# Performance work log

Hardware: AMD Instinct MI355X
Metric: run time of the kernel (lower is better)

## Reference

```python
import jax, jax.numpy as jnp
import numpy as np

B, M, K, P = 64, 8, 4, 16  # batch, rx antennas, streams, constellation size
NBPS = 4  # 16-QAM


def _qam_points(nbps):
    # square QAM, unit average energy
    n = 2 ** (nbps // 2)
    pam = 2.0 * np.arange(n) - n + 1.0  # e.g. {-3,-1,1,3}
    re, im = np.meshgrid(pam, pam, indexing='ij')
    pts = (re + 1j * im).reshape(-1)
    pts = pts / np.sqrt(np.mean(np.abs(pts) ** 2))
    return pts.astype(np.complex64)


def _build_vecs(points, k):
    # replicate MaximumLikelihoodDetector._build_vecs: stream 0 varies slowest
    p = points.shape[0]
    grids = np.meshgrid(*([np.arange(p)] * k), indexing='ij')
    idx = np.stack(grids, axis=-1).reshape(-1, k)        # [P^K, K]
    vecs = points[idx]                                   # [P^K, K] complex
    c = np.stack([
        np.stack([np.where(idx[:, j] == pi)[0] for j in range(k)], axis=-1)
        for pi in range(p)
    ], axis=-1)                                          # [P^(K-1), K, P]
    return vecs, c.astype(np.int32)


def setup_inputs() -> dict:
    key = jax.random.key(0)
    ks = jax.random.split(key, 6)
    points = _qam_points(NBPS)
    vecs, c = _build_vecs(points, K)
    yr = jax.random.normal(ks[0], (B, M), jnp.float32)
    yi = jax.random.normal(ks[1], (B, M), jnp.float32)
    hr = jax.random.normal(ks[2], (B, M, K), jnp.float32)
    hi = jax.random.normal(ks[3], (B, M, K), jnp.float32)
    # Hermitian positive-definite noise covariance s = A A^H / M + I
    ar = jax.random.normal(ks[4], (B, M, M), jnp.float32)
    ai = jax.random.normal(ks[5], (B, M, M), jnp.float32)
    a = (ar + 1j * ai).astype(jnp.complex64)
    s = a @ jnp.conj(jnp.swapaxes(a, -1, -2)) / M + jnp.eye(M, dtype=jnp.complex64)
    return {
        'yr': yr, 'yi': yi, 'hr': hr, 'hi': hi,
        'sr': jnp.real(s).astype(jnp.float32), 'si': jnp.imag(s).astype(jnp.float32),
        'vr': jnp.asarray(vecs.real), 'vi': jnp.asarray(vecs.imag),
        'c': jnp.asarray(c),
    }


def reference(yr, yi, hr, hi, sr, si, vr, vi, c):
    y = (yr + 1j * yi).astype(jnp.complex64)          # [B, M]
    h = (hr + 1j * hi).astype(jnp.complex64)          # [B, M, K]
    s = (sr + 1j * si).astype(jnp.complex64)          # [B, M, M]
    vecs = (vr + 1j * vi).astype(jnp.complex64)       # [V, K]
    # whitening: s_inv = inv(cholesky(s))
    L = jnp.linalg.cholesky(s)
    s_inv = jnp.linalg.inv(L)                         # [B, M, M]
    yw = jnp.einsum('bmn,bn->bm', s_inv, y)           # [B, M]
    hw = jnp.einsum('bmn,bnk->bmk', s_inv, h)         # [B, M, K]
    # distances for every candidate symbol vector
    hv = jnp.einsum('bmk,vk->bvm', hw, vecs)          # [B, V, M]
    diff = yw[:, None, :] - hv                        # [B, V, M]
    exponents = -jnp.sum(diff.real ** 2 + diff.imag ** 2, axis=-1)  # [B, V]
    # regroup exponents by (stream, symbol) and reduce (app -> logsumexp)
    exp_g = exponents[:, c]                           # [B, P^(K-1), K, P]
    logits = jax.nn.logsumexp(exp_g, axis=-3)         # [B, K, P]
    return logits
```

## Files before the change

### kernel.cpp

```cpp
#include <hip/hip_runtime.h>
#include <math.h>


__global__ __launch_bounds__(256) void k_main(
    const float* __restrict__ yr, const float* __restrict__ yi,
    const float* __restrict__ hr, const float* __restrict__ hi,
    const float* __restrict__ sr, const float* __restrict__ si,
    const float* __restrict__ vr, const float* __restrict__ vi,
    float* __restrict__ ws, float* __restrict__ out)
{
    __shared__ float sL[8][8][2];
    __shared__ float sDinv[8];
    __shared__ float lyw[8][2];
    __shared__ float lhw[8][4][2];
    __shared__ float tab[4][16][8][2];
    __shared__ float xbuf[16][256];
    __shared__ float pA[256], pB[256], pC[256];
    __shared__ float lmax[48];
    __shared__ float gsum[48];

    const int t = threadIdx.x;
    const int bid = blockIdx.x;
    const int b = bid >> 4, chunk = bid & 15;

    float Lr_[8], Li_[8], a_r[8], a_i[8];
    if (t < 8) {
#pragma unroll
        for (int k = 0; k < 8; ++k) {
            a_r[k] = sr[b * 64 + t * 8 + k];
            a_i[k] = si[b * 64 + t * 8 + k];
        }
    }
#pragma unroll
    for (int j = 0; j < 8; ++j) {
        if (t == j) {
            float d = a_r[j];
#pragma unroll
            for (int k = 0; k < 8; ++k) if (k < j) d -= Lr_[k]*Lr_[k] + Li_[k]*Li_[k];
            float ld = sqrtf(d);
            Lr_[j] = ld; Li_[j] = 0.f;
            sDinv[j] = 1.f / ld;
#pragma unroll
            for (int k = 0; k < 8; ++k) if (k <= j) { sL[j][k][0] = Lr_[k]; sL[j][k][1] = Li_[k]; }
        }
        __syncthreads();
        if (t < 8 && t > j) {
            float cr = a_r[j], ci = a_i[j];
#pragma unroll
            for (int k = 0; k < 8; ++k) if (k < j) {
                cr -= Lr_[k]*sL[j][k][0] + Li_[k]*sL[j][k][1];
                ci -= Li_[k]*sL[j][k][0] - Lr_[k]*sL[j][k][1];
            }
            float inv = sDinv[j];
            Lr_[j] = cr * inv; Li_[j] = ci * inv;
        }
    }
    if (t < 5) {
        float rr[8], ri[8], zr[8], zi[8];
        if (t == 0) {
#pragma unroll
            for (int i = 0; i < 8; ++i) { rr[i] = yr[b*8+i]; ri[i] = yi[b*8+i]; }
        } else {
#pragma unroll
            for (int i = 0; i < 8; ++i) { rr[i] = hr[(b*8+i)*4 + (t-1)]; ri[i] = hi[(b*8+i)*4 + (t-1)]; }
        }
#pragma unroll
        for (int i = 0; i < 8; ++i) {
            float cr = rr[i], ci = ri[i];
#pragma unroll
            for (int k = 0; k < 8; ++k) if (k < i) {
                cr -= sL[i][k][0]*zr[k] - sL[i][k][1]*zi[k];
                ci -= sL[i][k][0]*zi[k] + sL[i][k][1]*zr[k];
            }
            float inv = sDinv[i];
            zr[i] = cr * inv; zi[i] = ci * inv;
            if (t == 0) { lyw[i][0] = zr[i]; lyw[i][1] = zi[i]; }
            else        { lhw[i][t-1][0] = zr[i]; lhw[i][t-1][1] = zi[i]; }
        }
    }
    __syncthreads();

    for (int e = t; e < 512; e += 256) {
        int k = e >> 7, p = (e >> 3) & 15, m = e & 7;
        float hre = lhw[m][k][0], him = lhw[m][k][1];
        float pr = vr[(p << 12) * 4], pim = vi[(p << 12) * 4];
        tab[k][p][m][0] = hre*pr - him*pim;
        tab[k][p][m][1] = hre*pim + him*pr;
    }
    __syncthreads();

    const int i3 = t & 15, i2 = t >> 4;
    float br[8], bi[8];
#pragma unroll
    for (int m = 0; m < 8; ++m) {
        br[m] = tab[0][chunk][m][0] + tab[2][i2][m][0] + tab[3][i3][m][0] - lyw[m][0];
        bi[m] = tab[0][chunk][m][1] + tab[2][i2][m][1] + tab[3][i3][m][1] - lyw[m][1];
    }
#pragma unroll
    for (int s = 0; s < 16; ++s) {
        float acc = 0.f;
#pragma unroll
        for (int m = 0; m < 8; ++m) {
            float dr = br[m] + tab[1][s][m][0];
            float di = bi[m] + tab[1][s][m][1];
            acc += dr*dr + di*di;
        }
        xbuf[s][t] = -acc;
    }
    __syncthreads();

    float vmA = xbuf[0][t];
#pragma unroll
    for (int s = 1; s < 16; ++s) vmA = fmaxf(vmA, xbuf[s][t]);
    pA[t] = vmA;
    float vmB = xbuf[i2][i3];
#pragma unroll
    for (int d2 = 1; d2 < 16; ++d2) vmB = fmaxf(vmB, xbuf[i2][d2*16 + i3]);
    pB[t] = vmB;
    __syncthreads();
    if (t < 16) {
        float v1 = pB[t*16], v2 = pA[t*16], v3 = pA[t];
#pragma unroll
        for (int i = 1; i < 16; ++i) {
            v1 = fmaxf(v1, pB[t*16 + i]);
            v2 = fmaxf(v2, pA[t*16 + i]);
            v3 = fmaxf(v3, pA[t + 16*i]);
        }
        lmax[t] = v1; lmax[16+t] = v2; lmax[32+t] = v3;
    }
    __syncthreads();

    const float M1 = lmax[i2];
    const float M2 = lmax[16 + i2];
    const float M3 = lmax[32 + i3];
    float acc1 = 0.f, acc2 = 0.f, acc3 = 0.f;
#pragma unroll
    for (int s = 0; s < 16; ++s) {
        float v = xbuf[s][t];
        acc2 += __expf(v - M2);
        acc3 += __expf(v - M3);
    }
#pragma unroll
    for (int d2 = 0; d2 < 16; ++d2) {
        float w = xbuf[i2][d2*16 + i3];
        acc1 += __expf(w - M1);
    }
    pA[t] = acc2; pB[t] = acc3; pC[t] = acc1;
    __syncthreads();
    if (t < 16) {
        float s1 = 0.f, s2 = 0.f, s3 = 0.f;
#pragma unroll
        for (int i = 0; i < 16; ++i) {
            s1 += pC[t*16 + i];
            s2 += pA[t*16 + i];
            s3 += pB[t + 16*i];
        }
        gsum[t] = s1; gsum[16+t] = s2; gsum[32+t] = s3;
    }
    __syncthreads();

    if (t < 48) {
        float* w = ws + ((b*48 + t)*16 + chunk)*2;
        w[0] = lmax[t];
        w[1] = gsum[t];
    }
    if (t == 0) {
        float M = lmax[16];
#pragma unroll
        for (int i = 1; i < 16; ++i) M = fmaxf(M, lmax[16+i]);
        float S = 0.f;
#pragma unroll
        for (int i = 0; i < 16; ++i) S += gsum[16+i] * __expf(lmax[16+i] - M);
        out[b*64 + chunk] = logf(S) + M;
    }
}

__global__ __launch_bounds__(256) void k_comb(const float* __restrict__ ws, float* __restrict__ out)
{
    int idx = blockIdx.x * 256 + threadIdx.x;
    if (idx >= 64 * 48) return;
    int b = idx / 48, gi = idx % 48;
    const float* p = ws + (b*48 + gi)*32;
    float M = p[0];
#pragma unroll
    for (int i = 1; i < 16; ++i) M = fmaxf(M, p[2*i]);
    float S = 0.f;
#pragma unroll
    for (int i = 0; i < 16; ++i) S += p[2*i+1] * __expf(p[2*i] - M);
    out[b*64 + 16 + gi] = logf(S) + M;
}

extern "C" void kernel_launch(void* const* d_in, const int* in_sizes, int n_in,
                              void* d_out, int out_size, void* d_ws, size_t ws_size,
                              hipStream_t stream) {
    const float* yr = (const float*)d_in[0];
    const float* yi = (const float*)d_in[1];
    const float* hr = (const float*)d_in[2];
    const float* hi = (const float*)d_in[3];
    const float* sr = (const float*)d_in[4];
    const float* si = (const float*)d_in[5];
    const float* vr = (const float*)d_in[6];
    const float* vi = (const float*)d_in[7];
    float* ws = (float*)d_ws;
    float* out = (float*)d_out;
    hipLaunchKernelGGL(k_main, dim3(1024), dim3(256), 0, stream,
                       yr, yi, hr, hi, sr, si, vr, vi, ws, out);
    hipLaunchKernelGGL(k_comb, dim3(12), dim3(256), 0, stream, ws, out);
}
```

Baseline: 20.36 us.

## Restructure ML detector kernel with wave shuffles, expanded distance, and single-exp logsumexp

Cholesky factorization now runs inside one wavefront and uses lane shuffles instead of block-wide barriers. Distances are computed in expanded form (|b|^2 + |p|^2|h1|^2 + 2Re(b·t1)), so each candidate needs a dot product rather than a full squared difference. All 16 values stay in registers and the max/sum reductions use wave shuffles, so the shared xbuf and most __syncthreads calls are gone. One exp pass against min(M2,M3), rescaled afterwards, replaces the two separate exp loops. The expanded-distance form and the rescaling trick can lose floating-point accuracy or underflow when M2 and M3 are far apart.

```diff
diff --git a/kernel.cpp b/kernel.cpp
--- a/kernel.cpp
+++ b/kernel.cpp
@@ -13,165 +13,211 @@
     __shared__ float sDinv[8];
     __shared__ float lyw[8][2];
     __shared__ float lhw[8][4][2];
-    __shared__ float tab[4][16][8][2];
-    __shared__ float xbuf[16][256];
-    __shared__ float pA[256], pB[256], pC[256];
-    __shared__ float lmax[48];
-    __shared__ float gsum[48];
+    __shared__ float tab[4][8][16][2];
+    __shared__ float pn2b[16];
+    __shared__ float Hn1b;
+    __shared__ float m3w[4][16], s3w[4][16];
+    __shared__ float p1buf[16][16];
+    __shared__ float m1cbuf[16][16];
+    __shared__ float m2buf[16], s2buf[16];
 
     const int t = threadIdx.x;
-    const int bid = blockIdx.x;
-    const int b = bid >> 4, chunk = bid & 15;
-
-    float Lr_[8], Li_[8], a_r[8], a_i[8];
-    if (t < 8) {
-#pragma unroll
-        for (int k = 0; k < 8; ++k) {
-            a_r[k] = sr[b * 64 + t * 8 + k];
-            a_i[k] = si[b * 64 + t * 8 + k];
-        }
-    }
-#pragma unroll
-    for (int j = 0; j < 8; ++j) {
-        if (t == j) {
-            float d = a_r[j];
-#pragma unroll
-            for (int k = 0; k < 8; ++k) if (k < j) d -= Lr_[k]*Lr_[k] + Li_[k]*Li_[k];
-            float ld = sqrtf(d);
-            Lr_[j] = ld; Li_[j] = 0.f;
-            sDinv[j] = 1.f / ld;
-#pragma unroll
-            for (int k = 0; k < 8; ++k) if (k <= j) { sL[j][k][0] = Lr_[k]; sL[j][k][1] = Li_[k]; }
-        }
-        __syncthreads();
-        if (t < 8 && t > j) {
-            float cr = a_r[j], ci = a_i[j];
+    const int b = blockIdx.x >> 4, chunk = blockIdx.x & 15;
+    const int lane = t & 63, wv = t >> 6;
+    const int i3 = t & 15, i2 = t >> 4;
+
+    if (wv == 0) {
+        float ar_[8] = {}, ai_[8] = {}, Lr_[8] = {}, Li_[8] = {};
+        if (lane < 8) {
+#pragma unroll
+            for (int k = 0; k < 8; ++k) {
+                ar_[k] = sr[b * 64 + lane * 8 + k];
+                ai_[k] = si[b * 64 + lane * 8 + k];
+            }
+        }
+        float inv = 0.f;
+#pragma unroll
+        for (int j = 0; j < 8; ++j) {
+            if (lane == j) {
+                float d = ar_[j];
+#pragma unroll
+                for (int k = 0; k < 8; ++k) if (k < j) d -= Lr_[k]*Lr_[k] + Li_[k]*Li_[k];
+                float ld = sqrtf(d);
+                Lr_[j] = ld; Li_[j] = 0.f;
+                inv = 1.f / ld;
+                sDinv[j] = inv;
+            }
+            float invj = __shfl(inv, j);
+            float cr = ar_[j], ci = ai_[j];
 #pragma unroll
             for (int k = 0; k < 8; ++k) if (k < j) {
-                cr -= Lr_[k]*sL[j][k][0] + Li_[k]*sL[j][k][1];
-                ci -= Li_[k]*sL[j][k][0] - Lr_[k]*sL[j][k][1];
-            }
-            float inv = sDinv[j];
-            Lr_[j] = cr * inv; Li_[j] = ci * inv;
-        }
-    }
-    if (t < 5) {
-        float rr[8], ri[8], zr[8], zi[8];
-        if (t == 0) {
-#pragma unroll
-            for (int i = 0; i < 8; ++i) { rr[i] = yr[b*8+i]; ri[i] = yi[b*8+i]; }
-        } else {
-#pragma unroll
-            for (int i = 0; i < 8; ++i) { rr[i] = hr[(b*8+i)*4 + (t-1)]; ri[i] = hi[(b*8+i)*4 + (t-1)]; }
-        }
-#pragma unroll
-        for (int i = 0; i < 8; ++i) {
-            float cr = rr[i], ci = ri[i];
-#pragma unroll
-            for (int k = 0; k < 8; ++k) if (k < i) {
-                cr -= sL[i][k][0]*zr[k] - sL[i][k][1]*zi[k];
-                ci -= sL[i][k][0]*zi[k] + sL[i][k][1]*zr[k];
-            }
-            float inv = sDinv[i];
-            zr[i] = cr * inv; zi[i] = ci * inv;
-            if (t == 0) { lyw[i][0] = zr[i]; lyw[i][1] = zi[i]; }
-            else        { lhw[i][t-1][0] = zr[i]; lhw[i][t-1][1] = zi[i]; }
+                float Ljrk = __shfl(Lr_[k], j);
+                float Ljik = __shfl(Li_[k], j);
+                cr -= Lr_[k]*Ljrk + Li_[k]*Ljik;
+                ci -= Li_[k]*Ljrk - Lr_[k]*Ljik;
+            }
+            if (lane < 8 && lane > j) { Lr_[j] = cr * invj; Li_[j] = ci * invj; }
+        }
+        if (lane < 8) {
+#pragma unroll
+            for (int k = 0; k < 8; ++k) if (k <= lane) { sL[lane][k][0] = Lr_[k]; sL[lane][k][1] = Li_[k]; }
+        }
+        if (lane < 5) {
+            float rr[8], ri[8], zr[8], zi[8];
+            if (lane == 0) {
+#pragma unroll
+                for (int i = 0; i < 8; ++i) { rr[i] = yr[b*8+i]; ri[i] = yi[b*8+i]; }
+            } else {
+#pragma unroll
+                for (int i = 0; i < 8; ++i) { rr[i] = hr[(b*8+i)*4 + (lane-1)]; ri[i] = hi[(b*8+i)*4 + (lane-1)]; }
+            }
+#pragma unroll
+            for (int i = 0; i < 8; ++i) {
+                float cr = rr[i], ci = ri[i];
+#pragma unroll
+                for (int k = 0; k < 8; ++k) if (k < i) {
+                    cr -= sL[i][k][0]*zr[k] - sL[i][k][1]*zi[k];
+                    ci -= sL[i][k][0]*zi[k] + sL[i][k][1]*zr[k];
+                }
+                float dv = sDinv[i];
+                zr[i] = cr * dv; zi[i] = ci * dv;
+                if (lane == 0) { lyw[i][0] = zr[i]; lyw[i][1] = zi[i]; }
+                else           { lhw[i][lane-1][0] = zr[i]; lhw[i][lane-1][1] = zi[i]; }
+            }
+        }
+        {
+            int p = lane & 15;
+            float pr  = vr[(p << 12) * 4];
+            float pim = vi[(p << 12) * 4];
+            if (lane < 16) pn2b[lane] = pr*pr + pim*pim;
+            if (lane == 0) {
+                float hn = 0.f;
+#pragma unroll
+                for (int m = 0; m < 8; ++m) hn += lhw[m][1][0]*lhw[m][1][0] + lhw[m][1][1]*lhw[m][1][1];
+                Hn1b = hn;
+            }
+#pragma unroll
+            for (int it = 0; it < 8; ++it) {
+                int e = lane + it * 64;
+                int k = e >> 7, m = (e >> 4) & 7;
+                float hre = lhw[m][k][0], him = lhw[m][k][1];
+                tab[k][m][p][0] = hre*pr  - him*pim;
+                tab[k][m][p][1] = hre*pim + him*pr;
+            }
         }
     }
     __syncthreads();
 
-    for (int e = t; e < 512; e += 256) {
-        int k = e >> 7, p = (e >> 3) & 15, m = e & 7;
-        float hre = lhw[m][k][0], him = lhw[m][k][1];
-        float pr = vr[(p << 12) * 4], pim = vi[(p << 12) * 4];
-        tab[k][p][m][0] = hre*pr - him*pim;
-        tab[k][p][m][1] = hre*pim + him*pr;
+    float br_[8], bi_[8];
+    float B2 = 0.f;
+#pragma unroll
+    for (int m = 0; m < 8; ++m) {
+        const float2 t0 = *(const float2*)&tab[0][m][chunk][0];
+        const float2 t2 = *(const float2*)&tab[2][m][i2][0];
+        const float2 t3 = *(const float2*)&tab[3][m][i3][0];
+        const float2 yw = *(const float2*)&lyw[m][0];
+        br_[m] = t0.x + t2.x + t3.x - yw.x;
+        bi_[m] = t0.y + t2.y + t3.y - yw.y;
+        B2 = fmaf(br_[m], br_[m], fmaf(bi_[m], bi_[m], B2));
+    }
+    const float Hn1 = Hn1b;
+
+    float x_[16];
+    float vmA = -3.4e38f;
+#pragma unroll
+    for (int s = 0; s < 16; ++s) {
+        float D = 0.f;
+#pragma unroll
+        for (int m = 0; m < 8; ++m) {
+            const float2 t1 = *(const float2*)&tab[1][m][s][0];
+            D = fmaf(br_[m], t1.x, D);
+            D = fmaf(bi_[m], t1.y, D);
+        }
+        float x = fmaf(-2.f, D, -fmaf(pn2b[s], Hn1, B2));
+        x_[s] = x;
+        vmA = fmaxf(vmA, x);
+    }
+
+    float M2 = vmA;
+    M2 = fmaxf(M2, __shfl_xor(M2, 1));
+    M2 = fmaxf(M2, __shfl_xor(M2, 2));
+    M2 = fmaxf(M2, __shfl_xor(M2, 4));
+    M2 = fmaxf(M2, __shfl_xor(M2, 8));
+    float m3p = vmA;
+    m3p = fmaxf(m3p, __shfl_xor(m3p, 16));
+    m3p = fmaxf(m3p, __shfl_xor(m3p, 32));
+    if (lane < 16) m3w[wv][lane] = m3p;
+
+#pragma unroll
+    for (int s = 0; s < 16; ++s) {
+        float rcm = x_[s];
+        rcm = fmaxf(rcm, __shfl_xor(rcm, 1));
+        rcm = fmaxf(rcm, __shfl_xor(rcm, 2));
+        rcm = fmaxf(rcm, __shfl_xor(rcm, 4));
+        rcm = fmaxf(rcm, __shfl_xor(rcm, 8));
+        float e1 = __expf(x_[s] - rcm);
+        e1 += __shfl_xor(e1, 1);
+        e1 += __shfl_xor(e1, 2);
+        e1 += __shfl_xor(e1, 4);
+        e1 += __shfl_xor(e1, 8);
+        if (i3 == 0) { p1buf[s][i2] = e1; m1cbuf[s][i2] = rcm; }
     }
     __syncthreads();
 
-    const int i3 = t & 15, i2 = t >> 4;
-    float br[8], bi[8];
-#pragma unroll
-    for (int m = 0; m < 8; ++m) {
-        br[m] = tab[0][chunk][m][0] + tab[2][i2][m][0] + tab[3][i3][m][0] - lyw[m][0];
-        bi[m] = tab[0][chunk][m][1] + tab[2][i2][m][1] + tab[3][i3][m][1] - lyw[m][1];
-    }
-#pragma unroll
-    for (int s = 0; s < 16; ++s) {
-        float acc = 0.f;
-#pragma unroll
-        for (int m = 0; m < 8; ++m) {
-            float dr = br[m] + tab[1][s][m][0];
-            float di = bi[m] + tab[1][s][m][1];
-            acc += dr*dr + di*di;
-        }
-        xbuf[s][t] = -acc;
+    const float M3 = fmaxf(fmaxf(m3w[0][i3], m3w[1][i3]), fmaxf(m3w[2][i3], m3w[3][i3]));
+    const float Mlo = fminf(M2, M3);
+    float acc = 0.f;
+#pragma unroll
+    for (int s = 0; s < 16; ++s) acc += __expf(x_[s] - Mlo);
+    float acc2 = acc * __expf(Mlo - M2);
+    float acc3 = acc * __expf(Mlo - M3);
+    float S2 = acc2;
+    S2 += __shfl_xor(S2, 1);
+    S2 += __shfl_xor(S2, 2);
+    S2 += __shfl_xor(S2, 4);
+    S2 += __shfl_xor(S2, 8);
+    float s3p = acc3;
+    s3p += __shfl_xor(s3p, 16);
+    s3p += __shfl_xor(s3p, 32);
+    if (lane < 16) s3w[wv][lane] = s3p;
+    if (i3 == 0) {
+        m2buf[i2] = M2; s2buf[i2] = S2;
+        float* w = ws + ((b*48 + 16 + i2)*16 + chunk)*2;
+        w[0] = M2; w[1] = S2;
     }
     __syncthreads();
 
-    float vmA = xbuf[0][t];
-#pragma unroll
-    for (int s = 1; s < 16; ++s) vmA = fmaxf(vmA, xbuf[s][t]);
-    pA[t] = vmA;
-    float vmB = xbuf[i2][i3];
-#pragma unroll
-    for (int d2 = 1; d2 < 16; ++d2) vmB = fmaxf(vmB, xbuf[i2][d2*16 + i3]);
-    pB[t] = vmB;
-    __syncthreads();
+    {
+        float p1v = p1buf[i2][i3];
+        float m1c = m1cbuf[i2][i3];
+        float M1 = m1c;
+        M1 = fmaxf(M1, __shfl_xor(M1, 1));
+        M1 = fmaxf(M1, __shfl_xor(M1, 2));
+        M1 = fmaxf(M1, __shfl_xor(M1, 4));
+        M1 = fmaxf(M1, __shfl_xor(M1, 8));
+        float q = p1v * __expf(m1c - M1);
+        q += __shfl_xor(q, 1);
+        q += __shfl_xor(q, 2);
+        q += __shfl_xor(q, 4);
+        q += __shfl_xor(q, 8);
+        if (i3 == 0) {
+            float* w = ws + ((b*48 + i2)*16 + chunk)*2;
+            w[0] = M1; w[1] = q;
+        }
+    }
     if (t < 16) {
-        float v1 = pB[t*16], v2 = pA[t*16], v3 = pA[t];
-#pragma unroll
-        for (int i = 1; i < 16; ++i) {
-            v1 = fmaxf(v1, pB[t*16 + i]);
-            v2 = fmaxf(v2, pA[t*16 + i]);
-            v3 = fmaxf(v3, pA[t + 16*i]);
-        }
-        lmax[t] = v1; lmax[16+t] = v2; lmax[32+t] = v3;
-    }
-    __syncthreads();
-
-    const float M1 = lmax[i2];
-    const float M2 = lmax[16 + i2];
-    const float M3 = lmax[32 + i3];
-    float acc1 = 0.f, acc2 = 0.f, acc3 = 0.f;
-#pragma unroll
-    for (int s = 0; s < 16; ++s) {
-        float v = xbuf[s][t];
-        acc2 += __expf(v - M2);
-        acc3 += __expf(v - M3);
-    }
-#pragma unroll
-    for (int d2 = 0; d2 < 16; ++d2) {
-        float w = xbuf[i2][d2*16 + i3];
-        acc1 += __expf(w - M1);
-    }
-    pA[t] = acc2; pB[t] = acc3; pC[t] = acc1;
-    __syncthreads();
-    if (t < 16) {
-        float s1 = 0.f, s2 = 0.f, s3 = 0.f;
-#pragma unroll
-        for (int i = 0; i < 16; ++i) {
-            s1 += pC[t*16 + i];
-            s2 += pA[t*16 + i];
-            s3 += pB[t + 16*i];
-        }
-        gsum[t] = s1; gsum[16+t] = s2; gsum[32+t] = s3;
-    }
-    __syncthreads();
-
-    if (t < 48) {
-        float* w = ws + ((b*48 + t)*16 + chunk)*2;
-        w[0] = lmax[t];
-        w[1] = gsum[t];
+        float S3 = s3w[0][t] + s3w[1][t] + s3w[2][t] + s3w[3][t];
+        float* w = ws + ((b*48 + 32 + t)*16 + chunk)*2;
+        w[0] = M3; w[1] = S3;
     }
     if (t == 0) {
-        float M = lmax[16];
-#pragma unroll
-        for (int i = 1; i < 16; ++i) M = fmaxf(M, lmax[16+i]);
-        float S = 0.f;
-#pragma unroll
-        for (int i = 0; i < 16; ++i) S += gsum[16+i] * __expf(lmax[16+i] - M);
-        out[b*64 + chunk] = logf(S) + M;
+        float M0 = m2buf[0];
+#pragma unroll
+        for (int i = 1; i < 16; ++i) M0 = fmaxf(M0, m2buf[i]);
+        float S0 = 0.f;
+#pragma unroll
+        for (int i = 0; i < 16; ++i) S0 += s2buf[i] * __expf(m2buf[i] - M0);
+        out[b*64 + chunk] = __logf(S0) + M0;
     }
 }
 
@@ -187,7 +233,7 @@
     float S = 0.f;
 #pragma unroll
     for (int i = 0; i < 16; ++i) S += p[2*i+1] * __expf(p[2*i] - M);
-    out[b*64 + 16 + gi] = logf(S) + M;
+    out[b*64 + 16 + gi] = __logf(S) + M;
 }
 
 extern "C" void kernel_launch(void* const* d_in, const int* in_sizes, int n_in,
```

New measurement: 27.78 us. 1.36x slower.
